# Performance work log

Hardware: AMD Instinct MI355X
Metric: run time of the kernel (lower is better)

Reference implementation:

```python
import jax, jax.numpy as jnp
import numpy as np

B, D, T, C = 128, 128, 2048, 64


def setup_inputs() -> dict:
    key = jax.random.key(0)
    k1, k2, k3 = jax.random.split(key, 3)
    feature = jax.random.normal(k1, (B, D, T), dtype=jnp.float32)
    label = jax.random.randint(k2, (B, T), 0, C, dtype=jnp.int64)
    centers = jax.random.normal(k3, (C, D), dtype=jnp.float32)
    return {"feature": feature, "label": label, "centers": centers}


def reference(feature, label, centers):
    # feature: [B, D, T] -> flatten to [N, D] with N = B*T (transpose(2,1).reshape)
    num_classes, feat_dim = centers.shape
    feat = jnp.transpose(feature, (0, 2, 1)).reshape(-1, feat_dim)  # [N, D]
    lab = label.reshape(-1)                                          # [N]

    centers_batch = centers[lab]                                     # gather [N, D]
    center_loss = jnp.mean((feat - centers_batch) ** 2)              # MSELoss (mean)

    diff = centers_batch - feat                                      # [N, D]
    # scatter-sum of per-row diffs into their class slot (replaces python loop)
    difference = jax.ops.segment_sum(diff, lab, num_segments=num_classes)  # [C, D]
    appear_times = jnp.bincount(lab, length=num_classes)             # [C]
    difference = difference / jnp.clip(appear_times, 1, None).astype(difference.dtype)[:, None]
    return (center_loss, difference)
```

## Files before the change

kernel.cpp:

```cpp
#include <hip/hip_runtime.h>


#define NT 2048
#define NC 64

#define OFF_P     0
#define OFF_SSP   4194304
#define OFF_CNTP  4194816
#define OFF_CROSS 4227584
#define OFF_CC    4227616
#define OFF_SS    4227648

typedef __attribute__((ext_vector_type(8))) short bf16x8;
typedef __attribute__((ext_vector_type(4))) float f32x4;

__device__ __forceinline__ unsigned short bf16rne(float f) {
    unsigned int u = __float_as_uint(f);
    return (unsigned short)((u + 0x7FFFu + ((u >> 16) & 1u)) >> 16);
}

__global__ __launch_bounds__(256) void k_main(const float* __restrict__ feat,
                                              const int*  __restrict__ label,
                                              float* __restrict__ ws) {
    __shared__ int   labS[512];
    __shared__ int   cntS[NC];
    __shared__ float red[256];

    const int tid = threadIdx.x, bid = blockIdx.x;
    const int th = bid & 3, b = bid >> 2;
    const int wave = tid >> 6, lane = tid & 63;
    const int q = lane >> 4, q8 = q * 8, ln16 = lane & 15;
    const int wd0 = wave * 32;

    if (tid < NC) cntS[tid] = 0;
    __syncthreads();
    {
        const int2 L = *(const int2*)(label + b * NT + th * 512 + tid * 2);
        labS[tid * 2] = L.x; labS[tid * 2 + 1] = L.y;
        atomicAdd(&cntS[L.x], 1); atomicAdd(&cntS[L.y], 1);
    }
    __syncthreads();
    if (tid < NC) ((int*)(ws + OFF_CNTP))[bid * NC + tid] = cntS[tid];

    const float* pA0 = feat + ((size_t)(b * 128 + wd0 + ln16)) * NT + th * 512 + q8;
    const float* pA1 = pA0 + (size_t)16 * NT;

    f32x4 acc[2][4] = {};
    float ss = 0.0f;

    #pragma unroll 2
    for (int ks = 0; ks < 16; ++ks) {
        const int t0k = ks * 32;

        const float4 x0 = *(const float4*)(pA0 + t0k);
        const float4 x1 = *(const float4*)(pA0 + t0k + 4);
        const float4 y0 = *(const float4*)(pA1 + t0k);
        const float4 y1 = *(const float4*)(pA1 + t0k + 4);

        int labv[8];
        #pragma unroll
        for (int j = 0; j < 8; ++j) labv[j] = labS[t0k + q8 + j];

        ss += x0.x * x0.x + x0.y * x0.y + x0.z * x0.z + x0.w * x0.w
            + x1.x * x1.x + x1.y * x1.y + x1.z * x1.z + x1.w * x1.w
            + y0.x * y0.x + y0.y * y0.y + y0.z * y0.z + y0.w * y0.w
            + y1.x * y1.x + y1.y * y1.y + y1.z * y1.z + y1.w * y1.w;

        bf16x8 a0, a1;
        a0[0] = (short)bf16rne(x0.x); a0[1] = (short)bf16rne(x0.y);
        a0[2] = (short)bf16rne(x0.z); a0[3] = (short)bf16rne(x0.w);
        a0[4] = (short)bf16rne(x1.x); a0[5] = (short)bf16rne(x1.y);
        a0[6] = (short)bf16rne(x1.z); a0[7] = (short)bf16rne(x1.w);
        a1[0] = (short)bf16rne(y0.x); a1[1] = (short)bf16rne(y0.y);
        a1[2] = (short)bf16rne(y0.z); a1[3] = (short)bf16rne(y0.w);
        a1[4] = (short)bf16rne(y1.x); a1[5] = (short)bf16rne(y1.y);
        a1[6] = (short)bf16rne(y1.z); a1[7] = (short)bf16rne(y1.w);

        #pragma unroll
        for (int nt = 0; nt < 4; ++nt) {
            const int c_lane = nt * 16 + ln16;
            bf16x8 bo;
            #pragma unroll
            for (int j = 0; j < 8; ++j)
                bo[j] = (labv[j] == c_lane) ? (short)0x3F80 : (short)0;
            acc[0][nt] = __builtin_amdgcn_mfma_f32_16x16x32_bf16(a0, bo, acc[0][nt], 0, 0, 0);
            acc[1][nt] = __builtin_amdgcn_mfma_f32_16x16x32_bf16(a1, bo, acc[1][nt], 0, 0, 0);
        }
    }

    float* P = ws + OFF_P + (size_t)bid * 8192;
    #pragma unroll
    for (int mt = 0; mt < 2; ++mt)
        #pragma unroll
        for (int nt = 0; nt < 4; ++nt)
            #pragma unroll
            for (int r = 0; r < 4; ++r) {
                const int d = wd0 + mt * 16 + q * 4 + r;
                const int c = nt * 16 + ln16;
                P[d * 64 + c] = acc[mt][nt][r];
            }

    red[tid] = ss;
    __syncthreads();
    for (int s = 128; s > 0; s >>= 1) {
        if (tid < s) red[tid] += red[tid + s];
        __syncthreads();
    }
    if (tid == 0) ws[OFF_SSP + bid] = red[0];
}

__global__ __launch_bounds__(256) void k_red(float* __restrict__ ws,
                                             const float* __restrict__ centers,
                                             float* __restrict__ out) {
    const int tid = threadIdx.x, bid = blockIdx.x;

    if (bid == 32) {
        __shared__ float r[256];
        r[tid] = ws[OFF_SSP + tid] + ws[OFF_SSP + 256 + tid];
        __syncthreads();
        for (int k = 128; k > 0; k >>= 1) { if (tid < k) r[tid] += r[tid + k]; __syncthreads(); }
        if (tid == 0) ws[OFF_SS] = r[0];
        return;
    }

    __shared__ int cred[256];
    __shared__ int cnt[NC];
    {
        const int c = tid & 63, part = tid >> 6;
        const int* cntP = (const int*)(ws + OFF_CNTP);
        int s = 0;
        for (int e2 = part * 128; e2 < part * 128 + 128; ++e2) s += cntP[e2 * NC + c];
        cred[tid] = s;
    }
    __syncthreads();
    if (tid < NC) cnt[tid] = cred[tid] + cred[tid + 64] + cred[tid + 128] + cred[tid + 192];
    __syncthreads();

    const int i = bid * 256 + tid;
    const int d = i >> 6, c = i & 63;
    const float* Pp = ws + OFF_P + i;
    float sum = 0.0f;
    #pragma unroll 8
    for (int bb = 0; bb < 512; ++bb) sum += Pp[(size_t)bb * 8192];

    const float ctr = centers[c * 128 + d];
    const float cn  = (float)cnt[c];
    const float den = cn > 1.0f ? cn : 1.0f;
    out[1 + c * 128 + d] = (cn * ctr - sum) / den;

    __shared__ float r1[256], r2[256];
    r1[tid] = sum * ctr;
    r2[tid] = cn * ctr * ctr;
    __syncthreads();
    for (int k = 128; k > 0; k >>= 1) {
        if (tid < k) { r1[tid] += r1[tid + k]; r2[tid] += r2[tid + k]; }
        __syncthreads();
    }
    if (tid == 0) { ws[OFF_CROSS + bid] = r1[0]; ws[OFF_CC + bid] = r2[0]; }
}

__global__ __launch_bounds__(64) void k_epi(const float* __restrict__ ws,
                                            float* __restrict__ out) {
    int t = threadIdx.x;
    float cr = (t < 32) ? ws[OFF_CROSS + t] : 0.0f;
    float cc = (t < 32) ? ws[OFF_CC + t] : 0.0f;
    for (int o = 16; o > 0; o >>= 1) { cr += __shfl_down(cr, o); cc += __shfl_down(cc, o); }
    if (t == 0) out[0] = (ws[OFF_SS] - 2.0f * cr + cc) * (1.0f / 33554432.0f);
}

extern "C" void kernel_launch(void* const* d_in, const int* in_sizes, int n_in,
                              void* d_out, int out_size, void* d_ws, size_t ws_size,
                              hipStream_t stream) {
    const float* feat    = (const float*)d_in[0];
    const int*   label   = (const int*)d_in[1];
    const float* centers = (const float*)d_in[2];
    float* out = (float*)d_out;
    float* ws  = (float*)d_ws;

    hipLaunchKernelGGL(k_main, dim3(512), dim3(256), 0, stream, feat, label, ws);
    hipLaunchKernelGGL(k_red,  dim3(33),  dim3(256), 0, stream, ws, centers, out);
    hipLaunchKernelGGL(k_epi,  dim3(1),   dim3(64),  0, stream, ws, out);
}
```

Baseline: 244.0 us.

## Halve main-kernel blocks, software-prefetch feature loads, split partial reduction wider

```diff
diff --git a/kernel.cpp b/kernel.cpp
--- a/kernel.cpp
+++ b/kernel.cpp
@@ -5,11 +5,11 @@
 #define NC 64
 
 #define OFF_P     0
-#define OFF_SSP   4194304
-#define OFF_CNTP  4194816
-#define OFF_CROSS 4227584
-#define OFF_CC    4227616
-#define OFF_SS    4227648
+#define OFF_SSP   2097152
+#define OFF_CNTP  2097408
+#define OFF_CROSS 2113792
+#define OFF_CC    2113856
+#define OFF_SS    2113920
 
 typedef __attribute__((ext_vector_type(8))) short bf16x8;
 typedef __attribute__((ext_vector_type(4))) float f32x4;
@@ -22,12 +22,12 @@
 __global__ __launch_bounds__(256) void k_main(const float* __restrict__ feat,
                                               const int*  __restrict__ label,
                                               float* __restrict__ ws) {
-    __shared__ int   labS[512];
+    __shared__ int   labS[1024];
     __shared__ int   cntS[NC];
     __shared__ float red[256];
 
     const int tid = threadIdx.x, bid = blockIdx.x;
-    const int th = bid & 3, b = bid >> 2;
+    const int th = bid & 1, b = bid >> 1;
     const int wave = tid >> 6, lane = tid & 63;
     const int q = lane >> 4, q8 = q * 8, ln16 = lane & 15;
     const int wd0 = wave * 32;
@@ -35,57 +35,72 @@
     if (tid < NC) cntS[tid] = 0;
     __syncthreads();
     {
-        const int2 L = *(const int2*)(label + b * NT + th * 512 + tid * 2);
-        labS[tid * 2] = L.x; labS[tid * 2 + 1] = L.y;
+        const int4 L = *(const int4*)(label + b * NT + th * 1024 + tid * 4);
+        labS[tid * 4 + 0] = L.x; labS[tid * 4 + 1] = L.y;
+        labS[tid * 4 + 2] = L.z; labS[tid * 4 + 3] = L.w;
         atomicAdd(&cntS[L.x], 1); atomicAdd(&cntS[L.y], 1);
+        atomicAdd(&cntS[L.z], 1); atomicAdd(&cntS[L.w], 1);
     }
     __syncthreads();
     if (tid < NC) ((int*)(ws + OFF_CNTP))[bid * NC + tid] = cntS[tid];
 
-    const float* pA0 = feat + ((size_t)(b * 128 + wd0 + ln16)) * NT + th * 512 + q8;
+    const float* pA0 = feat + ((size_t)(b * 128 + wd0 + ln16)) * NT + th * 1024 + q8;
     const float* pA1 = pA0 + (size_t)16 * NT;
 
     f32x4 acc[2][4] = {};
     float ss = 0.0f;
 
-    #pragma unroll 2
-    for (int ks = 0; ks < 16; ++ks) {
+    float4 c0 = *(const float4*)(pA0);
+    float4 c1 = *(const float4*)(pA0 + 4);
+    float4 c2 = *(const float4*)(pA1);
+    float4 c3 = *(const float4*)(pA1 + 4);
+
+    #pragma unroll 4
+    for (int ks = 0; ks < 32; ++ks) {
         const int t0k = ks * 32;
-
-        const float4 x0 = *(const float4*)(pA0 + t0k);
-        const float4 x1 = *(const float4*)(pA0 + t0k + 4);
-        const float4 y0 = *(const float4*)(pA1 + t0k);
-        const float4 y1 = *(const float4*)(pA1 + t0k + 4);
-
-        int labv[8];
-        #pragma unroll
-        for (int j = 0; j < 8; ++j) labv[j] = labS[t0k + q8 + j];
-
-        ss += x0.x * x0.x + x0.y * x0.y + x0.z * x0.z + x0.w * x0.w
-            + x1.x * x1.x + x1.y * x1.y + x1.z * x1.z + x1.w * x1.w
-            + y0.x * y0.x + y0.y * y0.y + y0.z * y0.z + y0.w * y0.w
-            + y1.x * y1.x + y1.y * y1.y + y1.z * y1.z + y1.w * y1.w;
+        float4 n0, n1, n2, n3;
+        if (ks < 31) {
+            n0 = *(const float4*)(pA0 + t0k + 32);
+            n1 = *(const float4*)(pA0 + t0k + 36);
+            n2 = *(const float4*)(pA1 + t0k + 32);
+            n3 = *(const float4*)(pA1 + t0k + 36);
+        }
+
+        const int4 lv0 = *(const int4*)&labS[t0k + q8];
+        const int4 lv1 = *(const int4*)&labS[t0k + q8 + 4];
+
+        ss += c0.x * c0.x + c0.y * c0.y + c0.z * c0.z + c0.w * c0.w
+            + c1.x * c1.x + c1.y * c1.y + c1.z * c1.z + c1.w * c1.w
+            + c2.x * c2.x + c2.y * c2.y + c2.z * c2.z + c2.w * c2.w
+            + c3.x * c3.x + c3.y * c3.y + c3.z * c3.z + c3.w * c3.w;
 
         bf16x8 a0, a1;
-        a0[0] = (short)bf16rne(x0.x); a0[1] = (short)bf16rne(x0.y);
-        a0[2] = (short)bf16rne(x0.z); a0[3] = (short)bf16rne(x0.w);
-        a0[4] = (short)bf16rne(x1.x); a0[5] = (short)bf16rne(x1.y);
-        a0[6] = (short)bf16rne(x1.z); a0[7] = (short)bf16rne(x1.w);
-        a1[0] = (short)bf16rne(y0.x); a1[1] = (short)bf16rne(y0.y);
-        a1[2] = (short)bf16rne(y0.z); a1[3] = (short)bf16rne(y0.w);
-        a1[4] = (short)bf16rne(y1.x); a1[5] = (short)bf16rne(y1.y);
-        a1[6] = (short)bf16rne(y1.z); a1[7] = (short)bf16rne(y1.w);
+        a0[0] = (short)bf16rne(c0.x); a0[1] = (short)bf16rne(c0.y);
+        a0[2] = (short)bf16rne(c0.z); a0[3] = (short)bf16rne(c0.w);
+        a0[4] = (short)bf16rne(c1.x); a0[5] = (short)bf16rne(c1.y);
+        a0[6] = (short)bf16rne(c1.z); a0[7] = (short)bf16rne(c1.w);
+        a1[0] = (short)bf16rne(c2.x); a1[1] = (short)bf16rne(c2.y);
+        a1[2] = (short)bf16rne(c2.z); a1[3] = (short)bf16rne(c2.w);
+        a1[4] = (short)bf16rne(c3.x); a1[5] = (short)bf16rne(c3.y);
+        a1[6] = (short)bf16rne(c3.z); a1[7] = (short)bf16rne(c3.w);
 
         #pragma unroll
         for (int nt = 0; nt < 4; ++nt) {
             const int c_lane = nt * 16 + ln16;
             bf16x8 bo;
-            #pragma unroll
-            for (int j = 0; j < 8; ++j)
-                bo[j] = (labv[j] == c_lane) ? (short)0x3F80 : (short)0;
+            bo[0] = (lv0.x == c_lane) ? (short)0x3F80 : (short)0;
+            bo[1] = (lv0.y == c_lane) ? (short)0x3F80 : (short)0;
+            bo[2] = (lv0.z == c_lane) ? (short)0x3F80 : (short)0;
+            bo[3] = (lv0.w == c_lane) ? (short)0x3F80 : (short)0;
+            bo[4] = (lv1.x == c_lane) ? (short)0x3F80 : (short)0;
+            bo[5] = (lv1.y == c_lane) ? (short)0x3F80 : (short)0;
+            bo[6] = (lv1.z == c_lane) ? (short)0x3F80 : (short)0;
+            bo[7] = (lv1.w == c_lane) ? (short)0x3F80 : (short)0;
             acc[0][nt] = __builtin_amdgcn_mfma_f32_16x16x32_bf16(a0, bo, acc[0][nt], 0, 0, 0);
             acc[1][nt] = __builtin_amdgcn_mfma_f32_16x16x32_bf16(a1, bo, acc[1][nt], 0, 0, 0);
         }
+
+        c0 = n0; c1 = n1; c2 = n2; c3 = n3;
     }
 
     float* P = ws + OFF_P + (size_t)bid * 8192;
@@ -114,9 +129,9 @@
                                              float* __restrict__ out) {
     const int tid = threadIdx.x, bid = blockIdx.x;
 
-    if (bid == 32) {
+    if (bid == 64) {
         __shared__ float r[256];
-        r[tid] = ws[OFF_SSP + tid] + ws[OFF_SSP + 256 + tid];
+        r[tid] = ws[OFF_SSP + tid];
         __syncthreads();
         for (int k = 128; k > 0; k >>= 1) { if (tid < k) r[tid] += r[tid + k]; __syncthreads(); }
         if (tid == 0) ws[OFF_SS] = r[0];
@@ -129,28 +144,38 @@
         const int c = tid & 63, part = tid >> 6;
         const int* cntP = (const int*)(ws + OFF_CNTP);
         int s = 0;
-        for (int e2 = part * 128; e2 < part * 128 + 128; ++e2) s += cntP[e2 * NC + c];
+        #pragma unroll 8
+        for (int e2 = part * 64; e2 < part * 64 + 64; ++e2) s += cntP[e2 * NC + c];
         cred[tid] = s;
     }
     __syncthreads();
     if (tid < NC) cnt[tid] = cred[tid] + cred[tid + 64] + cred[tid + 128] + cred[tid + 192];
     __syncthreads();
 
-    const int i = bid * 256 + tid;
-    const int d = i >> 6, c = i & 63;
-    const float* Pp = ws + OFF_P + i;
+    const int el = tid & 127, half = tid >> 7;
+    const int e = bid * 128 + el;
+    const float* Pp = ws + OFF_P + (size_t)half * 128 * 8192 + e;
     float sum = 0.0f;
-    #pragma unroll 8
-    for (int bb = 0; bb < 512; ++bb) sum += Pp[(size_t)bb * 8192];
-
-    const float ctr = centers[c * 128 + d];
-    const float cn  = (float)cnt[c];
-    const float den = cn > 1.0f ? cn : 1.0f;
-    out[1 + c * 128 + d] = (cn * ctr - sum) / den;
+    #pragma unroll 16
+    for (int bb = 0; bb < 128; ++bb) sum += Pp[(size_t)bb * 8192];
+
+    __shared__ float sh[256];
+    sh[tid] = sum;
+    __syncthreads();
 
     __shared__ float r1[256], r2[256];
-    r1[tid] = sum * ctr;
-    r2[tid] = cn * ctr * ctr;
+    float v1 = 0.0f, v2 = 0.0f;
+    if (half == 0) {
+        const float tot = sh[el] + sh[el + 128];
+        const int d = e >> 6, c = e & 63;
+        const float ctr = centers[c * 128 + d];
+        const float cn  = (float)cnt[c];
+        const float den = cn > 1.0f ? cn : 1.0f;
+        out[1 + c * 128 + d] = (cn * ctr - tot) / den;
+        v1 = tot * ctr;
+        v2 = cn * ctr * ctr;
+    }
+    r1[tid] = v1; r2[tid] = v2;
     __syncthreads();
     for (int k = 128; k > 0; k >>= 1) {
         if (tid < k) { r1[tid] += r1[tid + k]; r2[tid] += r2[tid + k]; }
@@ -162,9 +187,10 @@
 __global__ __launch_bounds__(64) void k_epi(const float* __restrict__ ws,
                                             float* __restrict__ out) {
     int t = threadIdx.x;
-    float cr = (t < 32) ? ws[OFF_CROSS + t] : 0.0f;
-    float cc = (t < 32) ? ws[OFF_CC + t] : 0.0f;
-    for (int o = 16; o > 0; o >>= 1) { cr += __shfl_down(cr, o); cc += __shfl_down(cc, o); }
+    float cr = ws[OFF_CROSS + t];
+    float cc = ws[OFF_CC + t];
+    #pragma unroll
+    for (int o = 32; o > 0; o >>= 1) { cr += __shfl_down(cr, o); cc += __shfl_down(cc, o); }
     if (t == 0) out[0] = (ws[OFF_SS] - 2.0f * cr + cc) * (1.0f / 33554432.0f);
 }
 
@@ -177,7 +203,7 @@
     float* out = (float*)d_out;
     float* ws  = (float*)d_ws;
 
-    hipLaunchKernelGGL(k_main, dim3(512), dim3(256), 0, stream, feat, label, ws);
-    hipLaunchKernelGGL(k_red,  dim3(33),  dim3(256), 0, stream, ws, centers, out);
+    hipLaunchKernelGGL(k_main, dim3(256), dim3(256), 0, stream, feat, label, ws);
+    hipLaunchKernelGGL(k_red,  dim3(65),  dim3(256), 0, stream, ws, centers, out);
     hipLaunchKernelGGL(k_epi,  dim3(1),   dim3(64),  0, stream, ws, out);
 }
```

Measured after the change: 220.1 us. 9.8% less time.
